# Performance work log

Measured on AMD Instinct MI355X. Metric: run time of the kernel, lower is better.

## Reference

```python
import jax, jax.numpy as jnp
import numpy as np

BATCH = 131072
N = 64          # total bits
PARTS = 16      # len(partition) == dpp_size
M = 4           # bits per part
D = PARTS
EPS = 1e-8


def _colnorm(a):
    return a / jnp.linalg.norm(a, axis=0, keepdims=True)


def setup_inputs() -> dict:
    key = jax.random.key(0)
    k0, k1, k2, k3, k4 = jax.random.split(key, 5)
    x = jax.random.randint(k0, (BATCH, N), 0, 2, dtype=jnp.int32)
    W = jax.random.normal(k1, (PARTS, (1 << M) - 1), dtype=jnp.float32)
    A = _colnorm(jax.random.normal(k2, (D, D), dtype=jnp.float32))
    B = _colnorm(jax.random.normal(k3, (D, D), dtype=jnp.float32))
    C = _colnorm(jax.random.normal(k4, (D, D), dtype=jnp.float32))
    return {"x": x, "W": W, "A": A, "B": B, "C": C}


def reference(x, W, A, B, C):
    batch = x.shape[0]
    # --- Simple PCs (vectorized over the 16 parts): bit-pack each 4-bit part ---
    bits = x.reshape(batch, PARTS, M)                       # contiguous partition
    pow2 = (1 << jnp.arange(M)).astype(jnp.int32)           # [M]
    idx = jnp.sum(bits * pow2, axis=-1)                     # [B, P] in [0, 2^M)
    w = jax.nn.softmax(W, axis=-1)                          # [P, 2^M - 1]
    w = jnp.concatenate([jnp.zeros((PARTS, 1), w.dtype), w], axis=-1)  # [P, 2^M]
    p = w[jnp.arange(PARTS)[None, :], idx]                  # [B, P]

    # --- L matrix: sym PD part + skew part ---
    I = jnp.eye(D, dtype=A.dtype)
    L0 = A.T @ A + (B @ C.T - C @ B.T) + EPS * I            # [D, D]

    # column-scale by p, then force diagonal to 1 where p == 0
    Lp = L0[None, :, :] * p[:, None, :]                     # [B, D, D]
    eye_b = jnp.eye(D, dtype=bool)
    mask = eye_b[None, :, :] & (p == 0.0)[:, :, None]
    Lp = jnp.where(mask, jnp.asarray(1.0, Lp.dtype), Lp)

    sign, logabs = jnp.linalg.slogdet(Lp)                   # [B]
    y = logabs + jnp.log(jax.lax.stop_gradient(sign))       # nan if det < 0 (matches torch.logdet)
    s0, la0 = jnp.linalg.slogdet(L0 + I)
    alpha = la0 + jnp.log(jax.lax.stop_gradient(s0))
    return y - alpha
```

## Files before the change

kernel.cpp:

```cpp
#include <hip/hip_runtime.h>
#include <math.h>

#define BATCH 131072
#define EPS 1e-8f


__device__ __forceinline__ float lu_logdet(const float* sL0, unsigned m,
                                           float diagAdd) {
    float a[16][16];
    #pragma unroll
    for (int j = 0; j < 16; ++j) {
        bool on = (m >> j) & 1u;
        #pragma unroll
        for (int i = 0; i < 16; ++i) {
            float v = on ? sL0[i * 16 + j] : 0.f;
            if (i == j) v = on ? (v + diagAdd) : 1.f;
            a[i][j] = v;
        }
    }
    float logdet = 0.f;
    #pragma unroll
    for (int k = 0; k < 16; ++k) {
        float piv = a[k][k];
        logdet += __logf(fabsf(piv));
        float inv = 1.0f / piv;
        #pragma unroll
        for (int i2 = k + 1; i2 < 16; ++i2) {
            float f = a[i2][k] * inv;
            #pragma unroll
            for (int j2 = k + 1; j2 < 16; ++j2)
                a[i2][j2] = fmaf(-f, a[k][j2], a[i2][j2]);
        }
    }
    return logdet;
}

__global__ __launch_bounds__(64, 1) void table_kernel(
    const float* __restrict__ W, const float* __restrict__ A,
    const float* __restrict__ Bm, const float* __restrict__ Cm,
    float* __restrict__ ws) {
    __shared__ float sL0[256];
    int lt = threadIdx.x;

    #pragma unroll
    for (int q = 0; q < 4; ++q) {
        int e = lt * 4 + q;
        int i = e >> 4, j = e & 15;
        float s = 0.f;
        #pragma unroll
        for (int k = 0; k < 16; ++k) {
            s += A[k * 16 + i] * A[k * 16 + j];
            s += Bm[i * 16 + k] * Cm[j * 16 + k]
               - Cm[i * 16 + k] * Bm[j * 16 + k];
        }
        if (i == j) s += EPS;
        sL0[e] = s;
    }
    __syncthreads();

    unsigned blk = blockIdx.x;
    if (blk < 1024u) {
        unsigned m = blk * 64u + (unsigned)lt;
        ws[1024 + m] = lu_logdet(sL0, m, 0.f);
    } else {
        if (lt == 0) {
            ws[256] = lu_logdet(sL0, 0xFFFFu, 1.f);
        } else if (lt >= 32 && lt < 48) {
            int r = lt - 32;
            float row[15];
            float mx = -1e30f;
            #pragma unroll
            for (int q = 0; q < 15; ++q) {
                row[q] = W[r * 15 + q];
                mx = fmaxf(mx, row[q]);
            }
            float se = 0.f;
            #pragma unroll
            for (int q = 0; q < 15; ++q) se += expf(row[q] - mx);
            float lse = mx + logf(se);
            ws[r * 16 + 0] = 0.f;
            #pragma unroll
            for (int q = 0; q < 15; ++q) ws[r * 16 + 1 + q] = row[q] - lse;
        }
    }
}

__global__ __launch_bounds__(256) void main_kernel(const int4* __restrict__ x,
                                                   const float* __restrict__ ws,
                                                   float* __restrict__ out) {
    __shared__ float slw[256];
    int lt = threadIdx.x;
    slw[lt] = ws[lt];
    __syncthreads();

    int b = blockIdx.x * 256 + lt;
    const int4* xb = x + (size_t)b * 16;

    float lw = 0.f;
    unsigned mask = 0;
    #pragma unroll
    for (int j = 0; j < 16; ++j) {
        int4 v = xb[j];
        int idx = v.x + 2 * v.y + 4 * v.z + 8 * v.w;
        lw += slw[j * 16 + idx];
        mask |= (idx != 0 ? 1u : 0u) << j;
    }
    out[b] = lw + ws[1024 + mask] - ws[256];
}

extern "C" void kernel_launch(void* const* d_in, const int* in_sizes, int n_in,
                              void* d_out, int out_size, void* d_ws, size_t ws_size,
                              hipStream_t stream) {
    const int4*  x = (const int4*)d_in[0];
    const float* W = (const float*)d_in[1];
    const float* A = (const float*)d_in[2];
    const float* B = (const float*)d_in[3];
    const float* C = (const float*)d_in[4];
    float* ws  = (float*)d_ws;
    float* out = (float*)d_out;

    table_kernel<<<1025, 64, 0, stream>>>(W, A, B, C, ws);
    main_kernel<<<BATCH / 256, 256, 0, stream>>>(x, ws, out);
}
```

Before: 99.72 us.

## Replace 65536-entry determinant table with inverse-minor identity and overflow cleanup

Instead of precomputing LU log-determinants for all 65536 column masks, prep inverts L0 once and stores its log-determinant. Each sample then uses det(L0 restricted to active columns) = det(L0) * det(inverse restricted to inactive columns), computing a small closed-form determinant of at most 4x4. Samples with more than four zeroed parts are queued through an atomic counter and finished by a single-block cleanup kernel that runs a full masked LU. This removes the large table computation at the cost of an extra launch, an atomic on rare paths, a fixed overflow capacity, and possible accuracy loss from working with the inverse.

```diff
diff --git a/kernel.cpp b/kernel.cpp
--- a/kernel.cpp
+++ b/kernel.cpp
@@ -3,18 +3,18 @@
 
 #define BATCH 131072
 #define EPS 1e-8f
-
-
-__device__ __forceinline__ float lu_logdet(const float* sL0, unsigned m,
-                                           float diagAdd) {
+#define OVF_CAP 16384u
+
+
+__device__ __forceinline__ float lu_logdet_mask(const float* sMat, unsigned m) {
     float a[16][16];
     #pragma unroll
     for (int j = 0; j < 16; ++j) {
         bool on = (m >> j) & 1u;
         #pragma unroll
         for (int i = 0; i < 16; ++i) {
-            float v = on ? sL0[i * 16 + j] : 0.f;
-            if (i == j) v = on ? (v + diagAdd) : 1.f;
+            float v = on ? sMat[i * 16 + j] : 0.f;
+            if (i == j && !on) v = 1.f;
             a[i][j] = v;
         }
     }
@@ -35,17 +35,14 @@
     return logdet;
 }
 
-__global__ __launch_bounds__(64, 1) void table_kernel(
+__global__ __launch_bounds__(256) void prep_kernel(
     const float* __restrict__ W, const float* __restrict__ A,
     const float* __restrict__ Bm, const float* __restrict__ Cm,
     float* __restrict__ ws) {
     __shared__ float sL0[256];
-    int lt = threadIdx.x;
-
-    #pragma unroll
-    for (int q = 0; q < 4; ++q) {
-        int e = lt * 4 + q;
-        int i = e >> 4, j = e & 15;
+    int t = threadIdx.x;
+    {
+        int i = t >> 4, j = t & 15;
         float s = 0.f;
         #pragma unroll
         for (int k = 0; k < 16; ++k) {
@@ -54,43 +51,109 @@
                - Cm[i * 16 + k] * Bm[j * 16 + k];
         }
         if (i == j) s += EPS;
-        sL0[e] = s;
+        sL0[t] = s;
     }
     __syncthreads();
 
-    unsigned blk = blockIdx.x;
-    if (blk < 1024u) {
-        unsigned m = blk * 64u + (unsigned)lt;
-        ws[1024 + m] = lu_logdet(sL0, m, 0.f);
+    int w = t >> 6, lt = t & 63;
+    if (w == 0) {
+        float a[16][16];
+        #pragma unroll
+        for (int i = 0; i < 16; ++i)
+            #pragma unroll
+            for (int j = 0; j < 16; ++j) a[i][j] = sL0[i * 16 + j];
+        float logdet = 0.f;
+        #pragma unroll
+        for (int k = 0; k < 16; ++k) {
+            float piv = a[k][k];
+            logdet += __logf(fabsf(piv));
+            float inv = 1.0f / piv;
+            #pragma unroll
+            for (int i2 = k + 1; i2 < 16; ++i2) {
+                float f = a[i2][k] * inv;
+                a[i2][k] = f;
+                #pragma unroll
+                for (int j2 = k + 1; j2 < 16; ++j2)
+                    a[i2][j2] = fmaf(-f, a[k][j2], a[i2][j2]);
+            }
+        }
+        int c = lt & 15;
+        float y[16];
+        #pragma unroll
+        for (int i = 0; i < 16; ++i) {
+            float v = (i == c) ? 1.f : 0.f;
+            #pragma unroll
+            for (int k = 0; k < 16; ++k)
+                if (k < i) v = fmaf(-a[i][k], y[k], v);
+            y[i] = v;
+        }
+        float xc[16];
+        #pragma unroll
+        for (int i = 15; i >= 0; --i) {
+            float v = y[i];
+            #pragma unroll
+            for (int k = 0; k < 16; ++k)
+                if (k > i) v = fmaf(-a[i][k], xc[k], v);
+            xc[i] = v / a[i][i];
+        }
+        if (lt < 16) {
+            #pragma unroll
+            for (int i = 0; i < 16; ++i) ws[256 + i * 16 + c] = xc[i];
+        }
+        if (lt == 0) ws[512] = logdet;
+    } else if (w == 1) {
+        if (lt == 0) ws[513] = lu_logdet_mask(sL0, 0xFFFFu) == 0.f ? 0.f : 0.f;
+        float a[16][16];
+        #pragma unroll
+        for (int i = 0; i < 16; ++i)
+            #pragma unroll
+            for (int j = 0; j < 16; ++j)
+                a[i][j] = sL0[i * 16 + j] + ((i == j) ? 1.f : 0.f);
+        float logdet = 0.f;
+        #pragma unroll
+        for (int k = 0; k < 16; ++k) {
+            float piv = a[k][k];
+            logdet += __logf(fabsf(piv));
+            float inv = 1.0f / piv;
+            #pragma unroll
+            for (int i2 = k + 1; i2 < 16; ++i2) {
+                float f = a[i2][k] * inv;
+                #pragma unroll
+                for (int j2 = k + 1; j2 < 16; ++j2)
+                    a[i2][j2] = fmaf(-f, a[k][j2], a[i2][j2]);
+            }
+        }
+        if (lt == 0) ws[513] = logdet;
+    } else if (w == 2) {
+        int r = lt & 15;
+        float row[15];
+        float mx = -1e30f;
+        #pragma unroll
+        for (int q = 0; q < 15; ++q) {
+            row[q] = W[r * 15 + q];
+            mx = fmaxf(mx, row[q]);
+        }
+        float se = 0.f;
+        #pragma unroll
+        for (int q = 0; q < 15; ++q) se += expf(row[q] - mx);
+        float lse = mx + logf(se);
+        if (lt < 16) {
+            ws[r * 16 + 0] = 0.f;
+            #pragma unroll
+            for (int q = 0; q < 15; ++q) ws[r * 16 + 1 + q] = row[q] - lse;
+        }
     } else {
-        if (lt == 0) {
-            ws[256] = lu_logdet(sL0, 0xFFFFu, 1.f);
-        } else if (lt >= 32 && lt < 48) {
-            int r = lt - 32;
-            float row[15];
-            float mx = -1e30f;
-            #pragma unroll
-            for (int q = 0; q < 15; ++q) {
-                row[q] = W[r * 15 + q];
-                mx = fmaxf(mx, row[q]);
-            }
-            float se = 0.f;
-            #pragma unroll
-            for (int q = 0; q < 15; ++q) se += expf(row[q] - mx);
-            float lse = mx + logf(se);
-            ws[r * 16 + 0] = 0.f;
-            #pragma unroll
-            for (int q = 0; q < 15; ++q) ws[r * 16 + 1 + q] = row[q] - lse;
-        }
+        if (lt == 0) ((unsigned*)ws)[514] = 0u;
     }
 }
 
 __global__ __launch_bounds__(256) void main_kernel(const int4* __restrict__ x,
-                                                   const float* __restrict__ ws,
+                                                   float* __restrict__ ws,
                                                    float* __restrict__ out) {
-    __shared__ float slw[256];
+    __shared__ float s[512];
     int lt = threadIdx.x;
-    slw[lt] = ws[lt];
+    s[lt] = ws[lt];
+    s[256 + lt] = ws[256 + lt];
     __syncthreads();
 
     int b = blockIdx.x * 256 + lt;
@@ -102,10 +165,66 @@
     for (int j = 0; j < 16; ++j) {
         int4 v = xb[j];
         int idx = v.x + 2 * v.y + 4 * v.z + 8 * v.w;
-        lw += slw[j * 16 + idx];
+        lw += s[j * 16 + idx];
         mask |= (idx != 0 ? 1u : 0u) << j;
     }
-    out[b] = lw + ws[1024 + mask] - ws[256];
+    unsigned zb = (~mask) & 0xFFFFu;
+    int z = __popc(zb);
+    float base = lw + ws[512] - ws[513];
+
+    if (z <= 4) {
+        int zi[4];
+        unsigned tt = zb;
+        #pragma unroll
+        for (int q = 0; q < 4; ++q) {
+            zi[q] = tt ? (__ffs(tt) - 1) : 15;
+            tt &= tt - 1;
+        }
+        float m[4][4];
+        #pragma unroll
+        for (int r = 0; r < 4; ++r)
+            #pragma unroll
+            for (int c = 0; c < 4; ++c) {
+                float v = s[256 + zi[r] * 16 + zi[c]];
+                m[r][c] = (r < z && c < z) ? v : ((r == c) ? 1.f : 0.f);
+            }
+        float s0 = m[2][2] * m[3][3] - m[2][3] * m[3][2];
+        float s1 = m[2][1] * m[3][3] - m[2][3] * m[3][1];
+        float s2 = m[2][1] * m[3][2] - m[2][2] * m[3][1];
+        float s3 = m[2][0] * m[3][3] - m[2][3] * m[3][0];
+        float s4 = m[2][0] * m[3][2] - m[2][2] * m[3][0];
+        float s5 = m[2][0] * m[3][1] - m[2][1] * m[3][0];
+        float c0 = m[1][1] * s0 - m[1][2] * s1 + m[1][3] * s2;
+        float c1 = m[1][0] * s0 - m[1][2] * s3 + m[1][3] * s4;
+        float c2 = m[1][0] * s1 - m[1][1] * s3 + m[1][3] * s5;
+        float c3 = m[1][0] * s2 - m[1][1] * s4 + m[1][2] * s5;
+        float det = m[0][0] * c0 - m[0][1] * c1 + m[0][2] * c2 - m[0][3] * c3;
+        out[b] = base + __logf(fabsf(det));
+    } else {
+        unsigned pos = atomicAdd(((unsigned*)ws) + 514, 1u);
+        if (pos < OVF_CAP) {
+            ((int*)ws)[520 + 2 * pos] = b;
+            ((int*)ws)[521 + 2 * pos] = (int)zb;
+        }
+        out[b] = base;
+    }
+}
+
+__global__ __launch_bounds__(64) void cleanup_kernel(const float* __restrict__ ws,
+                                                     float* __restrict__ out) {
+    __shared__ float sM[256];
+    int lt = threadIdx.x;
+    #pragma unroll
+    for (int q = 0; q < 4; ++q) sM[lt * 4 + q] = ws[256 + lt * 4 + q];
+    __syncthreads();
+
+    unsigned n = ((const unsigned*)ws)[514];
+    if (n > OVF_CAP) n = OVF_CAP;
+    for (unsigned ii = (unsigned)lt; ii < n; ii += 64u) {
+        int b = ((const int*)ws)[520 + 2 * ii];
+        unsigned Z = (unsigned)((const int*)ws)[521 + 2 * ii];
+        out[b] += lu_logdet_mask(sM, Z);
+    }
 }
 
 extern "C" void kernel_launch(void* const* d_in, const int* in_sizes, int n_in,
@@ -119,6 +238,7 @@
     float* ws  = (float*)d_ws;
     float* out = (float*)d_out;
 
-    table_kernel<<<1025, 64, 0, stream>>>(W, A, B, C, ws);
+    prep_kernel<<<1, 256, 0, stream>>>(W, A, B, C, ws);
     main_kernel<<<BATCH / 256, 256, 0, stream>>>(x, ws, out);
-}
+    cleanup_kernel<<<1, 64, 0, stream>>>(ws, out);
+}
```

New measurement: 120.7 us. +21.0%, slower.
